# Kernel optimization log

Measured on AMD Instinct MI355X. Metric: run time of the kernel, lower is better.

The kernel has to match this reference:

```python
import jax, jax.numpy as jnp
import numpy as np

D_MODEL = 1024
NHEAD = 16
HEAD_DIM = D_MODEL // NHEAD
D_FF = 4096
BIAS_HID = 8
EPS = 1e-5


def _pair_bias(m, w1, b1, w2, b2):
    # m: [B,S,S] -> bias [B,S,S,nhead] via per-scalar MLP 1->hid->nhead
    h = jax.nn.relu(m[..., None] * w1 + b1)          # [B,S,S,hid]
    return jnp.einsum('bxyh,hn->bxyn', h, w2) + b2   # [B,S,S,nhead]


def _layernorm(x, g, b):
    mu = jnp.mean(x, axis=-1, keepdims=True)
    var = jnp.mean(jnp.square(x - mu), axis=-1, keepdims=True)
    return (x - mu) * jax.lax.rsqrt(var + EPS) * g + b


def setup_inputs() -> dict:
    key = jax.random.key(0)
    ks = jax.random.split(key, 20)
    B, S = 4, 1024
    sc = 1.0 / np.sqrt(D_MODEL)
    inp = {
        'src': jax.random.normal(ks[0], (B, S, D_MODEL), jnp.float32),
        't_deltas': jax.random.uniform(ks[1], (B, S, S), jnp.float32),
        'dists': jax.random.uniform(ks[2], (B, S, S), jnp.float32),
        'Wq': jax.random.normal(ks[3], (D_MODEL, D_MODEL), jnp.float32) * sc,
        'bq': jnp.zeros((D_MODEL,), jnp.float32),
        'Wk': jax.random.normal(ks[4], (D_MODEL, D_MODEL), jnp.float32) * sc,
        'bk': jnp.zeros((D_MODEL,), jnp.float32),
        'Wv': jax.random.normal(ks[5], (D_MODEL, D_MODEL), jnp.float32) * sc,
        'bv': jnp.zeros((D_MODEL,), jnp.float32),
        'tb_w1': jax.random.normal(ks[6], (BIAS_HID,), jnp.float32),
        'tb_b1': jnp.zeros((BIAS_HID,), jnp.float32),
        'tb_w2': jax.random.normal(ks[7], (BIAS_HID, NHEAD), jnp.float32) * 0.3,
        'tb_b2': jnp.zeros((NHEAD,), jnp.float32),
        'db_w1': jax.random.normal(ks[8], (BIAS_HID,), jnp.float32),
        'db_b1': jnp.zeros((BIAS_HID,), jnp.float32),
        'db_w2': jax.random.normal(ks[9], (BIAS_HID, NHEAD), jnp.float32) * 0.3,
        'db_b2': jnp.zeros((NHEAD,), jnp.float32),
        'W1': jax.random.normal(ks[10], (D_MODEL, D_FF), jnp.float32) * sc,
        'b1': jnp.zeros((D_FF,), jnp.float32),
        'W2': jax.random.normal(ks[11], (D_FF, D_MODEL), jnp.float32) / np.sqrt(D_FF),
        'b2': jnp.zeros((D_MODEL,), jnp.float32),
        'g1': jnp.ones((D_MODEL,), jnp.float32),
        'beta1': jnp.zeros((D_MODEL,), jnp.float32),
        'g2': jnp.ones((D_MODEL,), jnp.float32),
        'beta2': jnp.zeros((D_MODEL,), jnp.float32),
    }
    return inp


def reference(src, t_deltas, dists, Wq, bq, Wk, bk, Wv, bv,
              tb_w1, tb_b1, tb_w2, tb_b2, db_w1, db_b1, db_w2, db_b2,
              W1, b1, W2, b2, g1, beta1, g2, beta2):
    B, S, _ = src.shape
    # QKV projections -> [B, H, S, hd]
    q = (src @ Wq + bq).reshape(B, S, NHEAD, HEAD_DIM).transpose(0, 2, 1, 3)
    k = (src @ Wk + bk).reshape(B, S, NHEAD, HEAD_DIM).transpose(0, 2, 1, 3)
    v = (src @ Wv + bv).reshape(B, S, NHEAD, HEAD_DIM).transpose(0, 2, 1, 3)
    # scores scaled by sqrt(d_model) (as in the original, not head_dim)
    scores = jnp.einsum('bhqd,bhkd->bhqk', q, k) / jnp.sqrt(jnp.float32(D_MODEL))
    bias = (_pair_bias(t_deltas, tb_w1, tb_b1, tb_w2, tb_b2)
            + _pair_bias(dists, db_w1, db_b1, db_w2, db_b2))  # [B,S,S,H]
    scores = scores + bias.transpose(0, 3, 1, 2)
    attn = jax.nn.softmax(scores, axis=-1)
    out = jnp.einsum('bhqk,bhkd->bhqd', attn, v)
    out = out.transpose(0, 2, 1, 3).reshape(B, S, D_MODEL)
    x = _layernorm(src + out, g1, beta1)
    ffn = jax.nn.relu(x @ W1 + b1) @ W2 + b2
    return _layernorm(x + ffn, g2, beta2)
```

## Files before the change

kernel.cpp:

```cpp
#include <hip/hip_runtime.h>

typedef __bf16 bf16x8 __attribute__((ext_vector_type(8)));
typedef float f32x4 __attribute__((ext_vector_type(4)));
typedef unsigned short u16;

__device__ __forceinline__ u16 f2bf(float f) {
  union { float f; unsigned u; } x; x.f = f;
  unsigned r = x.u + 0x7fffu + ((x.u >> 16) & 1u);
  return (u16)(r >> 16);
}
__device__ __forceinline__ float bf2f(u16 u) {
  union { unsigned u; float f; } x; x.u = ((unsigned)u) << 16;
  return x.f;
}
__device__ __forceinline__ void gl_lds16(const void* g, void* l) {
  __builtin_amdgcn_global_load_lds(
      (const __attribute__((address_space(1))) void*)g,
      (__attribute__((address_space(3))) void*)l, 16, 0, 0);
}

__global__ __launch_bounds__(256) void cvt_kernel(const float* __restrict__ in,
                                                  u16* __restrict__ out, int n4) {
  int i = blockIdx.x * 256 + threadIdx.x;
  if (i >= n4) return;
  float4 v = ((const float4*)in)[i];
  unsigned lo = (unsigned)f2bf(v.x) | ((unsigned)f2bf(v.y) << 16);
  unsigned hi = (unsigned)f2bf(v.z) | ((unsigned)f2bf(v.w) << 16);
  uint2 u; u.x = lo; u.y = hi;
  *(uint2*)&out[(size_t)i * 4] = u;
}

__global__ __launch_bounds__(256) void tconv_kernel(const float* __restrict__ in,
                                                    u16* __restrict__ out, int R, int C) {
  __shared__ float tile[32][33];
  int c0 = blockIdx.x * 32, r0 = blockIdx.y * 32;
  int tx = threadIdx.x & 31, ty = threadIdx.x >> 5;
#pragma unroll
  for (int i = 0; i < 4; i++)
    tile[ty + i * 8][tx] = in[(size_t)(r0 + ty + i * 8) * C + c0 + tx];
  __syncthreads();
#pragma unroll
  for (int i = 0; i < 4; i++)
    out[(size_t)(c0 + ty + i * 8) * R + r0 + tx] = f2bf(tile[tx][ty + i * 8]);
}

__global__ __launch_bounds__(256) void bcat_kernel(const float* __restrict__ bq,
                                                   const float* __restrict__ bk,
                                                   const float* __restrict__ bv,
                                                   float* __restrict__ o) {
  int i = blockIdx.x * 256 + threadIdx.x;
  if (i >= 3072) return;
  o[i] = i < 1024 ? bq[i] : (i < 2048 ? bk[i - 1024] : bv[i - 2048]);
}

template <int EPI>
__global__ __launch_bounds__(512, 2) void gemm256_kernel(const u16* __restrict__ A,
                                                         const u16* __restrict__ Bt,
                                                         const float* __restrict__ bias,
                                                         void* __restrict__ out,
                                                         int M, int N, int K,
                                                         float qscale, int kslice) {
  __shared__ u16 lds[2][2][16384];
  int tid = threadIdx.x, w = tid >> 6, lane = tid & 63;
  int l16 = lane & 15, lhi = lane >> 4;
  int wr = w >> 2, wc = w & 3;
  int GX = gridDim.x;
  int nwg = GX * gridDim.y;
  int nlin = blockIdx.y * GX + blockIdx.x;
  int cpx = nwg >> 3;
  int sw = (nlin & 7) * cpx + (nlin >> 3);
  int m0 = (sw / GX) * 256, n0 = (sw % GX) * 256;
  int z = blockIdx.z;
  const u16* Ag = A + (size_t)m0 * K + z * kslice;
  const u16* Bg = Bt + (size_t)n0 * K + z * kslice;
  f32x4 acc[8][4] = {};
  const int c0q = (lhi ^ (l16 & 7)) << 3;
  const int c1q = ((4 | lhi) ^ (l16 & 7)) << 3;
  int nt = kslice >> 6;
  int r8 = lane >> 3;
  int gcol = 8 * ((lane & 7) ^ r8);

  auto stageHalf = [&](int p, int ab, int half, const u16* G) {
#pragma unroll
    for (int i = 0; i < 2; i++) {
      int r = half * 128 + i * 64 + w * 8 + r8;
      gl_lds16(G + (size_t)r * K + gcol,
               &lds[p][ab][(half * 128 + i * 64 + w * 8) * 64]);
    }
  };
  auto rdA = [&](int p, int mh, int cq, bf16x8* af) {
#pragma unroll
    for (int j = 0; j < 4; j++)
      af[j] = *(const bf16x8*)&lds[p][0][(mh * 128 + wr * 64 + j * 16 + l16) * 64 + cq];
  };
  auto rdB = [&](int p, int cq, bf16x8* bfr) {
#pragma unroll
    for (int nn = 0; nn < 4; nn++)
      bfr[nn] = *(const bf16x8*)&lds[p][1][(wc * 64 + nn * 16 + l16) * 64 + cq];
  };
  auto mma = [&](int mh, bf16x8* af, bf16x8* bfr) {
    __builtin_amdgcn_s_setprio(1);
#pragma unroll
    for (int j = 0; j < 4; j++)
#pragma unroll
      for (int nn = 0; nn < 4; nn++)
        acc[mh * 4 + j][nn] =
            __builtin_amdgcn_mfma_f32_16x16x32_bf16(af[j], bfr[nn], acc[mh * 4 + j][nn], 0, 0, 0);
    __builtin_amdgcn_s_setprio(0);
  };

  stageHalf(0, 1, 0, Bg);
  stageHalf(0, 0, 0, Ag);
  stageHalf(0, 1, 1, Bg);
  stageHalf(0, 0, 1, Ag);
  asm volatile("s_waitcnt vmcnt(2)" ::: "memory");
  __builtin_amdgcn_s_barrier();

  for (int t = 0; t < nt; ++t) {
    int p = t & 1, pn = p ^ 1;
    const u16* An = Ag + (t + 1) * 64;
    const u16* Bn = Bg + (t + 1) * 64;
    bool more = (t + 1 < nt);
    bf16x8 af[4], bfr[4];
    rdA(p, 0, c0q, af); rdB(p, c0q, bfr);
    if (more) { stageHalf(pn, 1, 0, Bn); stageHalf(pn, 0, 0, An); }
    mma(0, af, bfr);
    rdA(p, 0, c1q, af); rdB(p, c1q, bfr);
    if (more) {
      stageHalf(pn, 1, 1, Bn);
      asm volatile("s_waitcnt vmcnt(6)" ::: "memory");
    } else {
      asm volatile("s_waitcnt vmcnt(0)" ::: "memory");
    }
    __builtin_amdgcn_s_barrier();
    mma(0, af, bfr);
    rdA(p, 1, c0q, af); rdB(p, c0q, bfr);
    mma(1, af, bfr);
    rdA(p, 1, c1q, af); rdB(p, c1q, bfr);
    if (more) stageHalf(pn, 0, 1, An);
    mma(1, af, bfr);
    if (more) {
      asm volatile("s_waitcnt vmcnt(2)" ::: "memory");
      __builtin_amdgcn_s_barrier();
    }
  }

#pragma unroll
  for (int m = 0; m < 8; m++) {
    int gr = m0 + (m >> 2) * 128 + wr * 64 + (m & 3) * 16 + lhi * 4;
#pragma unroll
    for (int nn = 0; nn < 4; nn++) {
      int gc = n0 + wc * 64 + nn * 16 + l16;
      float bv;
      if (EPI == 0 || EPI == 3) bv = (z == 0 && bias) ? bias[gc] : 0.f;
      else bv = bias[gc];
      if (EPI == 2) {
        int seg = gc >> 10, c = gc & 1023, h = c >> 6, d = c & 63;
        float sc = (seg == 0) ? qscale : 1.f;
#pragma unroll
        for (int r = 0; r < 4; r++) {
          int row = gr + r;
          int b = row >> 10, s = row & 1023;
          size_t idx = ((((size_t)seg * 4 + b) * 16 + h) * 1024 + s) * 64 + d;
          ((u16*)out)[idx] = f2bf((acc[m][nn][r] + bv) * sc);
        }
      } else if (EPI == 1) {
#pragma unroll
        for (int r = 0; r < 4; r++)
          ((u16*)out)[(size_t)(gr + r) * N + gc] = f2bf(fmaxf(acc[m][nn][r] + bv, 0.f));
      } else if (EPI == 3) {
#pragma unroll
        for (int r = 0; r < 4; r++)
          ((u16*)out)[(size_t)z * M * N + (size_t)(gr + r) * N + gc] = f2bf(acc[m][nn][r] + bv);
      } else {
#pragma unroll
        for (int r = 0; r < 4; r++)
          ((float*)out)[(size_t)z * M * N + (size_t)(gr + r) * N + gc] = acc[m][nn][r] + bv;
      }
    }
  }
}

__global__ __launch_bounds__(256) void vtrans_kernel(const u16* __restrict__ v,
                                                     u16* __restrict__ vt) {
  __shared__ u16 t[64][72];
  int bh = blockIdx.y, s0 = blockIdx.x * 64;
  int tid = threadIdx.x;
  int r = tid >> 2, c = (tid & 3) * 16;
  const u16* src = v + ((size_t)bh * 1024 + s0 + r) * 64 + c;
  *(int4*)&t[r][c] = *(const int4*)src;
  *(int4*)&t[r][c + 8] = *(const int4*)(src + 8);
  __syncthreads();
  int d = tid >> 2, sc = (tid & 3) * 16;
  u16 tmp[16];
#pragma unroll
  for (int j = 0; j < 16; j++) tmp[j] = t[sc + j][d];
  u16* dst = vt + ((size_t)bh * 64 + d) * 1024 + s0 + sc;
  *(int4*)dst = *(int4*)&tmp[0];
  *(int4*)(dst + 8) = *(int4*)&tmp[8];
}

__global__ __launch_bounds__(256) void bias_kernel(
    const float* __restrict__ td, const float* __restrict__ dd,
    const float* __restrict__ tw1, const float* __restrict__ tb1,
    const float* __restrict__ tw2, const float* __restrict__ tb2,
    const float* __restrict__ dw1, const float* __restrict__ db1,
    const float* __restrict__ dw2, const float* __restrict__ db2,
    u16* __restrict__ biasout, int b0) {
  __shared__ float stw2[128], sdw2[128], sb2[16];
  __shared__ float stw1[8], stb1[8], sdw1[8], sdb1[8];
  int tid = threadIdx.x, x = blockIdx.x, bz = blockIdx.y;
  int b = b0 + bz;
  if (tid < 128) { stw2[tid] = tw2[tid]; sdw2[tid] = dw2[tid]; }
  if (tid < 16) sb2[tid] = tb2[tid] + db2[tid];
  if (tid < 8) { stw1[tid] = tw1[tid]; stb1[tid] = tb1[tid]; sdw1[tid] = dw1[tid]; sdb1[tid] = db1[tid]; }
  __syncthreads();
  float4 tv = ((const float4*)(td + ((size_t)b * 1024 + x) * 1024))[tid];
  float4 dv = ((const float4*)(dd + ((size_t)b * 1024 + x) * 1024))[tid];
  float tj[4] = {tv.x, tv.y, tv.z, tv.w};
  float dj[4] = {dv.x, dv.y, dv.z, dv.w};
  float ht[4][8], hd[4][8];
#pragma unroll
  for (int j = 0; j < 4; j++)
#pragma unroll
    for (int i = 0; i < 8; i++) {
      ht[j][i] = fmaxf(tj[j] * stw1[i] + stb1[i], 0.f);
      hd[j][i] = fmaxf(dj[j] * sdw1[i] + sdb1[i], 0.f);
    }
  u16* outb = biasout + (size_t)bz * 16 * 1024 * 1024 + (size_t)x * 1024 + tid * 4;
#pragma unroll
  for (int h = 0; h < 16; h++) {
    float a[4];
#pragma unroll
    for (int j = 0; j < 4; j++) {
      float s = sb2[h];
#pragma unroll
      for (int i = 0; i < 8; i++)
        s += ht[j][i] * stw2[i * 16 + h] + hd[j][i] * sdw2[i * 16 + h];
      a[j] = s;
    }
    unsigned lo = (unsigned)f2bf(a[0]) | ((unsigned)f2bf(a[1]) << 16);
    unsigned hi = (unsigned)f2bf(a[2]) | ((unsigned)f2bf(a[3]) << 16);
    uint2 u; u.x = lo; u.y = hi;
    *(uint2*)&outb[(size_t)h * 1024 * 1024] = u;
  }
}

#define LDA 72
__global__ __launch_bounds__(256) void attn_kernel(
    const u16* __restrict__ qg, const u16* __restrict__ kg, const u16* __restrict__ vtg,
    const u16* __restrict__ bias, float* __restrict__ attn_out, int b0) {
  __shared__ u16 Ks[64 * LDA];
  __shared__ u16 Vt[64 * LDA];
  __shared__ u16 Ps[64 * LDA];
  int tid = threadIdx.x;
  int w = tid >> 6, l = tid & 63, l16 = l & 15, lhi = l >> 4;
  int qt = blockIdx.x, h = blockIdx.y, bz = blockIdx.z;
  int b = b0 + bz;
  size_t bh = ((size_t)(b * 16 + h)) * 1024 * 64;
  const u16* biasb = bias + (size_t)bz * 16 * 1024 * 1024 + (size_t)h * 1024 * 1024;
  int qrow = qt * 64 + w * 16 + l16;
  bf16x8 qa[2];
  qa[0] = *(const bf16x8*)&qg[bh + (size_t)qrow * 64 + lhi * 8];
  qa[1] = *(const bf16x8*)&qg[bh + (size_t)qrow * 64 + 32 + lhi * 8];

  float m_run[4], l_run[4];
  f32x4 o[4] = {};
#pragma unroll
  for (int r = 0; r < 4; r++) { m_run[r] = -1e30f; l_run[r] = 0.f; }

  int kr0 = (tid * 2) >> 3, kc0 = ((tid * 2) & 7) * 8;
  int kr1 = (tid * 2 + 1) >> 3, kc1 = ((tid * 2 + 1) & 7) * 8;

  for (int kt = 0; kt < 16; kt++) {
    __syncthreads();
    *(int4*)&Ks[kr0 * LDA + kc0] = *(const int4*)&kg[bh + (size_t)(kt * 64 + kr0) * 64 + kc0];
    *(int4*)&Ks[kr1 * LDA + kc1] = *(const int4*)&kg[bh + (size_t)(kt * 64 + kr1) * 64 + kc1];
    *(int4*)&Vt[kr0 * LDA + kc0] = *(const int4*)&vtg[bh + (size_t)kr0 * 1024 + kt * 64 + kc0];
    *(int4*)&Vt[kr1 * LDA + kc1] = *(const int4*)&vtg[bh + (size_t)kr1 * 1024 + kt * 64 + kc1];
    __syncthreads();

    f32x4 s[4] = {};
    __builtin_amdgcn_s_setprio(1);
#pragma unroll
    for (int ni = 0; ni < 4; ni++)
#pragma unroll
      for (int ks = 0; ks < 2; ks++) {
        bf16x8 kb = *(const bf16x8*)&Ks[(ni * 16 + l16) * LDA + ks * 32 + lhi * 8];
        s[ni] = __builtin_amdgcn_mfma_f32_16x16x32_bf16(qa[ks], kb, s[ni], 0, 0, 0);
      }
    __builtin_amdgcn_s_setprio(0);
#pragma unroll
    for (int ni = 0; ni < 4; ni++)
#pragma unroll
      for (int r = 0; r < 4; r++) {
        int brow = qt * 64 + w * 16 + lhi * 4 + r;
        s[ni][r] += bf2f(biasb[(size_t)brow * 1024 + kt * 64 + ni * 16 + l16]);
      }
    float rs[4];
#pragma unroll
    for (int r = 0; r < 4; r++) {
      float m = fmaxf(fmaxf(s[0][r], s[1][r]), fmaxf(s[2][r], s[3][r]));
      m = fmaxf(m, __shfl_xor(m, 1, 16));
      m = fmaxf(m, __shfl_xor(m, 2, 16));
      m = fmaxf(m, __shfl_xor(m, 4, 16));
      m = fmaxf(m, __shfl_xor(m, 8, 16));
      float m2 = fmaxf(m_run[r], m);
      float sc = __expf(m_run[r] - m2);
      float sum = 0.f;
#pragma unroll
      for (int ni = 0; ni < 4; ni++) {
        float p = __expf(s[ni][r] - m2);
        s[ni][r] = p;
        sum += p;
      }
      sum += __shfl_xor(sum, 1, 16);
      sum += __shfl_xor(sum, 2, 16);
      sum += __shfl_xor(sum, 4, 16);
      sum += __shfl_xor(sum, 8, 16);
      l_run[r] = l_run[r] * sc + sum;
      m_run[r] = m2;
      rs[r] = sc;
    }
#pragma unroll
    for (int di = 0; di < 4; di++)
#pragma unroll
      for (int r = 0; r < 4; r++)
        o[di][r] *= rs[r];
#pragma unroll
    for (int ni = 0; ni < 4; ni++)
#pragma unroll
      for (int r = 0; r < 4; r++)
        Ps[(w * 16 + lhi * 4 + r) * LDA + ni * 16 + l16] = f2bf(s[ni][r]);
    __builtin_amdgcn_s_setprio(1);
#pragma unroll
    for (int ks = 0; ks < 2; ks++) {
      bf16x8 pa = *(const bf16x8*)&Ps[(w * 16 + l16) * LDA + ks * 32 + lhi * 8];
#pragma unroll
      for (int di = 0; di < 4; di++) {
        bf16x8 vb = *(const bf16x8*)&Vt[(di * 16 + l16) * LDA + ks * 32 + lhi * 8];
        o[di] = __builtin_amdgcn_mfma_f32_16x16x32_bf16(pa, vb, o[di], 0, 0, 0);
      }
    }
    __builtin_amdgcn_s_setprio(0);
  }
#pragma unroll
  for (int r = 0; r < 4; r++) {
    float inv = 1.f / l_run[r];
    int row = b * 1024 + qt * 64 + w * 16 + lhi * 4 + r;
#pragma unroll
    for (int di = 0; di < 4; di++)
      attn_out[(size_t)row * 1024 + h * 64 + di * 16 + l16] = o[di][r] * inv;
  }
}

__global__ __launch_bounds__(256) void ln_kernel(const float* __restrict__ a,
                                                 const float* __restrict__ r1,
                                                 const float* __restrict__ g,
                                                 const float* __restrict__ beta,
                                                 float* __restrict__ outf,
                                                 u16* __restrict__ outbf) {
  int row = blockIdx.x, tid = threadIdx.x;
  __shared__ float red[8];
  float4 va = ((const float4*)(a + (size_t)row * 1024))[tid];
  float4 vr = ((const float4*)(r1 + (size_t)row * 1024))[tid];
  float v[4] = {va.x + vr.x, va.y + vr.y, va.z + vr.z, va.w + vr.w};
  float s = v[0] + v[1] + v[2] + v[3];
#pragma unroll
  for (int off = 32; off >= 1; off >>= 1) s += __shfl_xor(s, off, 64);
  if ((tid & 63) == 0) red[tid >> 6] = s;
  __syncthreads();
  float mean = (red[0] + red[1] + red[2] + red[3]) * (1.f / 1024.f);
  float q = 0.f;
#pragma unroll
  for (int j = 0; j < 4; j++) { float d = v[j] - mean; q += d * d; }
#pragma unroll
  for (int off = 32; off >= 1; off >>= 1) q += __shfl_xor(q, off, 64);
  if ((tid & 63) == 0) red[4 + (tid >> 6)] = q;
  __syncthreads();
  float var = (red[4] + red[5] + red[6] + red[7]) * (1.f / 1024.f);
  float rstd = rsqrtf(var + 1e-5f);
  float4 gv = ((const float4*)g)[tid];
  float4 bv = ((const float4*)beta)[tid];
  float o0 = (v[0] - mean) * rstd * gv.x + bv.x;
  float o1 = (v[1] - mean) * rstd * gv.y + bv.y;
  float o2 = (v[2] - mean) * rstd * gv.z + bv.z;
  float o3 = (v[3] - mean) * rstd * gv.w + bv.w;
  float4 ov; ov.x = o0; ov.y = o1; ov.z = o2; ov.w = o3;
  ((float4*)(outf + (size_t)row * 1024))[tid] = ov;
  unsigned lo = (unsigned)f2bf(o0) | ((unsigned)f2bf(o1) << 16);
  unsigned hi = (unsigned)f2bf(o2) | ((unsigned)f2bf(o3) << 16);
  uint2 u; u.x = lo; u.y = hi;
  *(uint2*)&outbf[(size_t)row * 1024 + tid * 4] = u;
}

__global__ __launch_bounds__(256) void ln2_kernel(const float* __restrict__ x,
                                                  const u16* __restrict__ ff, int zs,
                                                  const float* __restrict__ g,
                                                  const float* __restrict__ beta,
                                                  float* __restrict__ out) {
  int row = blockIdx.x, tid = threadIdx.x;
  __shared__ float red[8];
  float4 xv = ((const float4*)(x + (size_t)row * 1024))[tid];
  float v[4] = {xv.x, xv.y, xv.z, xv.w};
  for (int z = 0; z < zs; z++) {
    uint2 u = *(const uint2*)&ff[(size_t)z * 4096 * 1024 + (size_t)row * 1024 + tid * 4];
    v[0] += bf2f(u.x & 0xffff); v[1] += bf2f(u.x >> 16);
    v[2] += bf2f(u.y & 0xffff); v[3] += bf2f(u.y >> 16);
  }
  float s = v[0] + v[1] + v[2] + v[3];
#pragma unroll
  for (int off = 32; off >= 1; off >>= 1) s += __shfl_xor(s, off, 64);
  if ((tid & 63) == 0) red[tid >> 6] = s;
  __syncthreads();
  float mean = (red[0] + red[1] + red[2] + red[3]) * (1.f / 1024.f);
  float q = 0.f;
#pragma unroll
  for (int j = 0; j < 4; j++) { float d = v[j] - mean; q += d * d; }
#pragma unroll
  for (int off = 32; off >= 1; off >>= 1) q += __shfl_xor(q, off, 64);
  if ((tid & 63) == 0) red[4 + (tid >> 6)] = q;
  __syncthreads();
  float var = (red[4] + red[5] + red[6] + red[7]) * (1.f / 1024.f);
  float rstd = rsqrtf(var + 1e-5f);
  float4 gv = ((const float4*)g)[tid];
  float4 bv = ((const float4*)beta)[tid];
  float4 ov;
  ov.x = (v[0] - mean) * rstd * gv.x + bv.x;
  ov.y = (v[1] - mean) * rstd * gv.y + bv.y;
  ov.z = (v[2] - mean) * rstd * gv.z + bv.z;
  ov.w = (v[3] - mean) * rstd * gv.w + bv.w;
  ((float4*)(out + (size_t)row * 1024))[tid] = ov;
}

extern "C" void kernel_launch(void* const* d_in, const int* in_sizes, int n_in,
                              void* d_out, int out_size, void* d_ws, size_t ws_size,
                              hipStream_t stream) {
  const float* src      = (const float*)d_in[0];
  const float* t_deltas = (const float*)d_in[1];
  const float* dists    = (const float*)d_in[2];
  const float* Wq = (const float*)d_in[3];
  const float* bq = (const float*)d_in[4];
  const float* Wk = (const float*)d_in[5];
  const float* bk = (const float*)d_in[6];
  const float* Wv = (const float*)d_in[7];
  const float* bv = (const float*)d_in[8];
  const float* tb_w1 = (const float*)d_in[9];
  const float* tb_b1 = (const float*)d_in[10];
  const float* tb_w2 = (const float*)d_in[11];
  const float* tb_b2 = (const float*)d_in[12];
  const float* db_w1 = (const float*)d_in[13];
  const float* db_b1 = (const float*)d_in[14];
  const float* db_w2 = (const float*)d_in[15];
  const float* db_b2 = (const float*)d_in[16];
  const float* W1 = (const float*)d_in[17];
  const float* b1 = (const float*)d_in[18];
  const float* W2 = (const float*)d_in[19];
  const float* b2 = (const float*)d_in[20];
  const float* g1 = (const float*)d_in[21];
  const float* beta1 = (const float*)d_in[22];
  const float* g2 = (const float*)d_in[23];
  const float* beta2 = (const float*)d_in[24];
  float* out = (float*)d_out;

  const size_t MB = 1024u * 1024;
  bool big = ws_size >= 150 * MB;
  int PB = big ? 2 : 1;
  int ZS = big ? 4 : 2;

  char* ws = (char*)d_ws;
  size_t off = 0;
  auto alloc = [&](size_t n) { void* p = ws + off; off += (n + 255) & ~(size_t)255; return p; };
  u16* src_bf  = (u16*)alloc(4096u * 1024 * 2);
  u16* wqkv_bt = (u16*)alloc(3072u * 1024 * 2);
  u16* w1_bt   = (u16*)alloc(4096u * 1024 * 2);
  u16* w2_bt   = (u16*)alloc(1024u * 4096 * 2);
  float* bcat  = (float*)alloc(3072u * 4);
  u16* qkv     = (u16*)alloc(3u * 4 * 16 * 1024 * 64 * 2);
  u16* vt      = (u16*)alloc(4u * 16 * 64 * 1024 * 2);
  u16* slab    = (u16*)alloc((size_t)PB * 16 * 1024 * 1024 * 2);
  float* attn_out = (float*)alloc(4096u * 1024 * 4);
  (void)in_sizes; (void)n_in; (void)out_size;

  u16* q_bf = qkv;
  u16* k_bf = qkv + 4u * 16 * 1024 * 64;
  u16* v_bf = qkv + 8u * 16 * 1024 * 64;
  float* x_f32 = (float*)qkv;
  u16*   x_bf  = (u16*)((char*)qkv + 16 * MB);
  u16*   h_bf  = (u16*)vt;
  u16*   ffnb  = big ? (u16*)((char*)slab + 24 * MB)
                     : (u16*)attn_out;

  cvt_kernel<<<4096, 256, 0, stream>>>(src, src_bf, 4096 * 1024 / 4);
  tconv_kernel<<<dim3(32, 32), 256, 0, stream>>>(Wq, wqkv_bt, 1024, 1024);
  tconv_kernel<<<dim3(32, 32), 256, 0, stream>>>(Wk, wqkv_bt + 1024u * 1024, 1024, 1024);
  tconv_kernel<<<dim3(32, 32), 256, 0, stream>>>(Wv, wqkv_bt + 2048u * 1024, 1024, 1024);
  tconv_kernel<<<dim3(128, 32), 256, 0, stream>>>(W1, w1_bt, 1024, 4096);
  tconv_kernel<<<dim3(32, 128), 256, 0, stream>>>(W2, w2_bt, 4096, 1024);
  bcat_kernel<<<12, 256, 0, stream>>>(bq, bk, bv, bcat);

  gemm256_kernel<2><<<dim3(12, 16, 1), 512, 0, stream>>>(src_bf, wqkv_bt, bcat, qkv,
                                                         4096, 3072, 1024, 1.f / 32.f, 1024);
  vtrans_kernel<<<dim3(16, 64), 256, 0, stream>>>(v_bf, vt);

  for (int p = 0; p < 4 / PB; p++) {
    bias_kernel<<<dim3(1024, PB), 256, 0, stream>>>(t_deltas, dists, tb_w1, tb_b1, tb_w2, tb_b2,
                                                    db_w1, db_b1, db_w2, db_b2, slab, p * PB);
    attn_kernel<<<dim3(16, 16, PB), 256, 0, stream>>>(q_bf, k_bf, vt, slab, attn_out, p * PB);
  }

  ln_kernel<<<4096, 256, 0, stream>>>(src, attn_out, g1, beta1, x_f32, x_bf);
  gemm256_kernel<1><<<dim3(16, 16, 1), 512, 0, stream>>>(x_bf, w1_bt, b1, h_bf,
                                                         4096, 4096, 1024, 1.f, 1024);
  gemm256_kernel<3><<<dim3(4, 16, ZS), 512, 0, stream>>>(h_bf, w2_bt, b2, ffnb,
                                                         4096, 1024, 4096, 1.f, 4096 / ZS);
  ln2_kernel<<<4096, 256, 0, stream>>>(x_f32, ffnb, ZS, g2, beta2, out);
}
```

Before: 300.6 us.

## Restructure GEMM mainloop into 8-phase ping-pong schedule with K-split LDS halves

Rewrites the 256x256 bf16 GEMM main loop so each 64-wide K tile is stored as two 32-wide halves with a new XOR swizzle. Each iteration now covers two K tiles in eight phases, and every phase issues one global-to-LDS stage, reads LDS fragments, then runs an MFMA block between barriers with raised priority. Each wave now owns a contiguous 128-row M slab rather than two interleaved 64-row halves, and the epilogue row mapping is updated to match. The aim is finer overlap of global loads, LDS reads and MFMA. In exchange it adds many more barriers per K step, and it appears to assume kslice is a multiple of 128.

```diff
diff --git a/kernel.cpp b/kernel.cpp
--- a/kernel.cpp
+++ b/kernel.cpp
@@ -60,7 +60,7 @@
                                                          void* __restrict__ out,
                                                          int M, int N, int K,
                                                          float qscale, int kslice) {
-  __shared__ u16 lds[2][2][16384];
+  __shared__ u16 lds[2][2][2][8192];
   int tid = threadIdx.x, w = tid >> 6, lane = tid & 63;
   int l16 = lane & 15, lhi = lane >> 4;
   int wr = w >> 2, wc = w & 3;
@@ -74,80 +74,97 @@
   const u16* Ag = A + (size_t)m0 * K + z * kslice;
   const u16* Bg = Bt + (size_t)n0 * K + z * kslice;
   f32x4 acc[8][4] = {};
-  const int c0q = (lhi ^ (l16 & 7)) << 3;
-  const int c1q = ((4 | lhi) ^ (l16 & 7)) << 3;
-  int nt = kslice >> 6;
-  int r8 = lane >> 3;
-  int gcol = 8 * ((lane & 7) ^ r8);
-
-  auto stageHalf = [&](int p, int ab, int half, const u16* G) {
-#pragma unroll
-    for (int i = 0; i < 2; i++) {
-      int r = half * 128 + i * 64 + w * 8 + r8;
-      gl_lds16(G + (size_t)r * K + gcol,
-               &lds[p][ab][(half * 128 + i * 64 + w * 8) * 64]);
-    }
+  int niter = kslice >> 7;
+
+  int srow0 = tid >> 2;
+  int sxor = ((tid & 3) ^ ((tid >> 3) & 3)) * 8;
+  int rga = (lhi ^ ((l16 >> 1) & 3)) * 8;
+
+  auto stage = [&](int buf, int op, int kh, const u16* Gt) {
+#pragma unroll
+    for (int ld = 0; ld < 2; ld++)
+      gl_lds16(Gt + (size_t)(ld * 128 + srow0) * K + kh * 32 + sxor,
+               &lds[buf][op][kh][ld * 4096 + w * 512]);
   };
-  auto rdA = [&](int p, int mh, int cq, bf16x8* af) {
+  auto rdA = [&](int buf, int kh, int mq, bf16x8* af) {
 #pragma unroll
     for (int j = 0; j < 4; j++)
-      af[j] = *(const bf16x8*)&lds[p][0][(mh * 128 + wr * 64 + j * 16 + l16) * 64 + cq];
+      af[j] = *(const bf16x8*)&lds[buf][0][kh][(wr * 128 + mq * 64 + j * 16 + l16) * 32 + rga];
   };
-  auto rdB = [&](int p, int cq, bf16x8* bfr) {
+  auto rdB = [&](int buf, int kh, bf16x8* bfr) {
 #pragma unroll
     for (int nn = 0; nn < 4; nn++)
-      bfr[nn] = *(const bf16x8*)&lds[p][1][(wc * 64 + nn * 16 + l16) * 64 + cq];
+      bfr[nn] = *(const bf16x8*)&lds[buf][1][kh][(wc * 64 + nn * 16 + l16) * 32 + rga];
   };
-  auto mma = [&](int mh, bf16x8* af, bf16x8* bfr) {
+  auto mma16 = [&](int mq, bf16x8* af, bf16x8* bfr) {
     __builtin_amdgcn_s_setprio(1);
 #pragma unroll
     for (int j = 0; j < 4; j++)
 #pragma unroll
       for (int nn = 0; nn < 4; nn++)
-        acc[mh * 4 + j][nn] =
-            __builtin_amdgcn_mfma_f32_16x16x32_bf16(af[j], bfr[nn], acc[mh * 4 + j][nn], 0, 0, 0);
+        acc[mq * 4 + j][nn] =
+            __builtin_amdgcn_mfma_f32_16x16x32_bf16(af[j], bfr[nn], acc[mq * 4 + j][nn], 0, 0, 0);
     __builtin_amdgcn_s_setprio(0);
   };
 
-  stageHalf(0, 1, 0, Bg);
-  stageHalf(0, 0, 0, Ag);
-  stageHalf(0, 1, 1, Bg);
-  stageHalf(0, 0, 1, Ag);
-  asm volatile("s_waitcnt vmcnt(2)" ::: "memory");
+#define PH_TAIL(MQ)                                          \
+  __builtin_amdgcn_s_barrier();                              \
+  asm volatile("s_waitcnt lgkmcnt(0)" ::: "memory");         \
+  __builtin_amdgcn_sched_barrier(0);                         \
+  mma16(MQ, af, bfr);                                        \
   __builtin_amdgcn_s_barrier();
 
-  for (int t = 0; t < nt; ++t) {
-    int p = t & 1, pn = p ^ 1;
-    const u16* An = Ag + (t + 1) * 64;
-    const u16* Bn = Bg + (t + 1) * 64;
-    bool more = (t + 1 < nt);
+  stage(0, 0, 0, Ag);       stage(0, 1, 0, Bg);
+  stage(0, 0, 1, Ag);       stage(0, 1, 1, Bg);
+  stage(1, 0, 0, Ag + 64);  stage(1, 1, 0, Bg + 64);
+  asm volatile("s_waitcnt vmcnt(4)" ::: "memory");
+  __builtin_amdgcn_s_barrier();
+
+  for (int j = 0; j < niter; ++j) {
+    const u16* A1 = Ag + (size_t)(2 * j + 1) * 64;
+    const u16* B1 = Bg + (size_t)(2 * j + 1) * 64;
+    const u16* A2 = Ag + (size_t)(2 * j + 2) * 64;
+    const u16* B2 = Bg + (size_t)(2 * j + 2) * 64;
+    bool more = (j + 1 < niter);
     bf16x8 af[4], bfr[4];
-    rdA(p, 0, c0q, af); rdB(p, c0q, bfr);
-    if (more) { stageHalf(pn, 1, 0, Bn); stageHalf(pn, 0, 0, An); }
-    mma(0, af, bfr);
-    rdA(p, 0, c1q, af); rdB(p, c1q, bfr);
+    rdA(0, 0, 0, af); rdB(0, 0, bfr);
+    stage(1, 0, 1, A1);
+    PH_TAIL(0)
+    rdA(0, 0, 1, af);
+    stage(1, 1, 1, B1);
+    PH_TAIL(1)
+    rdA(0, 1, 0, af); rdB(0, 1, bfr);
+    if (more) stage(0, 0, 0, A2);
+    PH_TAIL(0)
+    rdA(0, 1, 1, af);
     if (more) {
-      stageHalf(pn, 1, 1, Bn);
-      asm volatile("s_waitcnt vmcnt(6)" ::: "memory");
+      stage(0, 1, 0, B2);
+      asm volatile("s_waitcnt vmcnt(4)" ::: "memory");
     } else {
       asm volatile("s_waitcnt vmcnt(0)" ::: "memory");
     }
-    __builtin_amdgcn_s_barrier();
-    mma(0, af, bfr);
-    rdA(p, 1, c0q, af); rdB(p, c0q, bfr);
-    mma(1, af, bfr);
-    rdA(p, 1, c1q, af); rdB(p, c1q, bfr);
-    if (more) stageHalf(pn, 0, 1, An);
-    mma(1, af, bfr);
+    PH_TAIL(1)
+    rdA(1, 0, 0, af); rdB(1, 0, bfr);
+    if (more) stage(0, 0, 1, A2);
+    PH_TAIL(0)
+    rdA(1, 0, 1, af);
+    if (more) stage(0, 1, 1, B2);
+    PH_TAIL(1)
+    rdA(1, 1, 0, af); rdB(1, 1, bfr);
+    if (more) stage(1, 0, 0, A2 + 64);
+    PH_TAIL(0)
+    rdA(1, 1, 1, af);
     if (more) {
-      asm volatile("s_waitcnt vmcnt(2)" ::: "memory");
-      __builtin_amdgcn_s_barrier();
-    }
-  }
+      stage(1, 1, 0, B2 + 64);
+      asm volatile("s_waitcnt vmcnt(4)" ::: "memory");
+    }
+    PH_TAIL(1)
+  }
+#undef PH_TAIL
 
 #pragma unroll
   for (int m = 0; m < 8; m++) {
-    int gr = m0 + (m >> 2) * 128 + wr * 64 + (m & 3) * 16 + lhi * 4;
+    int gr = m0 + wr * 128 + (m >> 2) * 64 + (m & 3) * 16 + lhi * 4;
 #pragma unroll
     for (int nn = 0; nn < 4; nn++) {
       int gc = n0 + wc * 64 + nn * 16 + l16;
```

Result: no change. 297.0 us (-1.2%).
